# Optimization experiments

Hardware: AMD Instinct MI355X
Metric: run time of the kernel (lower is better)

Reference implementation:

```python
import jax, jax.numpy as jnp
import numpy as np
from jax import lax

C_IN, C_OUT, KH, KW = 8, 8, 3, 3
H, W = 2048, 2048


def setup_inputs() -> dict:
    key = jax.random.key(0)
    k_x, k_w = jax.random.split(key)
    x = jax.random.normal(k_x, (C_IN, H, W), dtype=jnp.float32)
    # kaiming-uniform-ish init, bound = 1/sqrt(fan_in)
    bound = 1.0 / np.sqrt(C_IN * KH * KW)
    weight = jax.random.uniform(k_w, (C_OUT, C_IN, KH, KW), dtype=jnp.float32,
                                minval=-bound, maxval=bound)
    return {"x": x, "weight": weight}


def reference(x, weight):
    # Faithful to Conv2d_mvm_function.forward: valid cross-correlation on a
    # single (C,H,W) image; stride/padding/dilation ignored, bias never added.
    out = lax.conv_general_dilated(
        x[None],                      # (1, C_in, H, W)
        weight,                       # (C_out, C_in, KH, KW)
        window_strides=(1, 1),
        padding="VALID",
        dimension_numbers=("NCHW", "OIHW", "NCHW"),
    )
    return out[0]                     # (C_out, H-KH+1, W-KW+1)
```

## Files before the change

### kernel.cpp

```cpp
#include <hip/hip_runtime.h>


#define H_IN   2048
#define W_IN   2048
#define H_OUT  2046
#define W_OUT  2046
#define CIN    8
#define COUT   8

#define TPR 512
#define NGROUPS 1023
#define PLANE ((size_t)H_IN * W_IN)

__device__ __forceinline__
void load_rows(float (&in)[4][6], const float* __restrict__ base, int ci, bool full) {
    #pragma unroll
    for (int r = 0; r < 4; ++r) {
        const float* p = base + (size_t)ci * PLANE + (size_t)r * W_IN;
        const float4 v4 = *reinterpret_cast<const float4*>(p);
        in[r][0] = v4.x; in[r][1] = v4.y; in[r][2] = v4.z; in[r][3] = v4.w;
        if (full) {
            const float2 v2 = *reinterpret_cast<const float2*>(p + 4);
            in[r][4] = v2.x; in[r][5] = v2.y;
        } else {
            in[r][4] = 0.0f; in[r][5] = 0.0f;
        }
    }
}

__device__ __forceinline__
void compute_ci(float (&acc)[2][COUT][4], const float (&in)[4][6],
                const float* __restrict__ w, int ci) {
    #pragma unroll
    for (int r = 0; r < 4; ++r) {
        #pragma unroll
        for (int co = 0; co < COUT; ++co) {
            #pragma unroll
            for (int kw = 0; kw < 3; ++kw) {
                if (r < 3) {
                    const float wt = w[((co * CIN + ci) * 3 + r) * 3 + kw];
                    #pragma unroll
                    for (int px = 0; px < 4; ++px)
                        acc[0][co][px] = fmaf(wt, in[r][kw + px], acc[0][co][px]);
                }
                if (r >= 1) {
                    const float wt = w[((co * CIN + ci) * 3 + (r - 1)) * 3 + kw];
                    #pragma unroll
                    for (int px = 0; px < 4; ++px)
                        acc[1][co][px] = fmaf(wt, in[r][kw + px], acc[1][co][px]);
                }
            }
        }
    }
}

__global__ __launch_bounds__(256)
void conv3x3_v3(const float* __restrict__ x,
                const float* __restrict__ w,
                float* __restrict__ out) {
    const int gtid = blockIdx.x * 256 + threadIdx.x;
    const int g  = gtid / TPR;
    const int tw = gtid - g * TPR;
    const int oh = g * 2;
    const int ow = tw * 4;
    const bool full = (tw != TPR - 1);

    float acc[2][COUT][4];
    #pragma unroll
    for (int r = 0; r < 2; ++r)
        #pragma unroll
        for (int co = 0; co < COUT; ++co)
            #pragma unroll
            for (int p = 0; p < 4; ++p)
                acc[r][co][p] = 0.0f;

    const float* base = x + (size_t)oh * W_IN + ow;

    float A[4][6], B[4][6];
    load_rows(A, base, 0, full);

    #pragma unroll 1
    for (int k = 0; k < CIN / 2; ++k) {
        const int ci0 = 2 * k;
        const int ci1 = ci0 + 1;

        load_rows(B, base, ci1, full);
        __builtin_amdgcn_sched_barrier(0);
        compute_ci(acc, A, w, ci0);

        if (k < CIN / 2 - 1)
            load_rows(A, base, ci0 + 2, full);
        __builtin_amdgcn_sched_barrier(0);
        compute_ci(acc, B, w, ci1);
    }

    #pragma unroll
    for (int co = 0; co < COUT; ++co) {
        float* o0 = out + ((size_t)co * H_OUT + (size_t)oh) * W_OUT + ow;
        float* o1 = o0 + W_OUT;
        if (full) {
            *reinterpret_cast<float4*>(o0) =
                make_float4(acc[0][co][0], acc[0][co][1], acc[0][co][2], acc[0][co][3]);
            *reinterpret_cast<float2*>(o1)     = make_float2(acc[1][co][0], acc[1][co][1]);
            *reinterpret_cast<float2*>(o1 + 2) = make_float2(acc[1][co][2], acc[1][co][3]);
        } else {
            *reinterpret_cast<float2*>(o0) = make_float2(acc[0][co][0], acc[0][co][1]);
            *reinterpret_cast<float2*>(o1) = make_float2(acc[1][co][0], acc[1][co][1]);
        }
    }
}

extern "C" void kernel_launch(void* const* d_in, const int* in_sizes, int n_in,
                              void* d_out, int out_size, void* d_ws, size_t ws_size,
                              hipStream_t stream) {
    const float* x = (const float*)d_in[0];
    const float* w = (const float*)d_in[1];
    float* out = (float*)d_out;

    const int total_threads = NGROUPS * TPR;
    const int block = 256;
    const int grid = total_threads / block;

    conv3x3_v3<<<grid, block, 0, stream>>>(x, w, out);
}
```

Measured before the change: 278.0 us.

## Stage input rows in LDS via async global_load_lds with double buffering

Each 512-thread block now handles two output rows across the full width. The four input rows per channel are staged into a double-buffered LDS tile with direct global-to-LDS loads, and explicit vmcnt waits plus barriers let the next channel load while the current one is computed. The aim is to replace the overlapping unaligned global float4/float2 reads with coalesced 16-byte async copies and to overlap memory with compute. It adds 64KB of LDS per block, which limits occupancy, and block-wide barrier synchronisation, and it relies on hand-tuned waitcnt counts being correct.

```diff
diff --git a/kernel.cpp b/kernel.cpp
--- a/kernel.cpp
+++ b/kernel.cpp
@@ -1,4 +1,5 @@
 #include <hip/hip_runtime.h>
+#include <stdint.h>
 
 
 #define H_IN   2048
@@ -7,30 +8,29 @@
 #define W_OUT  2046
 #define CIN    8
 #define COUT   8
+#define PLANE  ((size_t)H_IN * W_IN)
 
-#define TPR 512
-#define NGROUPS 1023
-#define PLANE ((size_t)H_IN * W_IN)
+template<int N>
+__device__ __forceinline__ void vm_wait() {
+    asm volatile("s_waitcnt vmcnt(%0)" :: "n"(N) : "memory");
+}
 
 __device__ __forceinline__
-void load_rows(float (&in)[4][6], const float* __restrict__ base, int ci, bool full) {
+void compute_phase(float (&acc)[2][COUT][4],
+                   const float* __restrict__ w, int ci,
+                   const float (&buf)[4][W_IN], int ow, bool full) {
+    float in[4][6];
     #pragma unroll
     for (int r = 0; r < 4; ++r) {
-        const float* p = base + (size_t)ci * PLANE + (size_t)r * W_IN;
-        const float4 v4 = *reinterpret_cast<const float4*>(p);
+        const float4 v4 = *reinterpret_cast<const float4*>(&buf[r][ow]);
         in[r][0] = v4.x; in[r][1] = v4.y; in[r][2] = v4.z; in[r][3] = v4.w;
         if (full) {
-            const float2 v2 = *reinterpret_cast<const float2*>(p + 4);
+            const float2 v2 = *reinterpret_cast<const float2*>(&buf[r][ow + 4]);
             in[r][4] = v2.x; in[r][5] = v2.y;
         } else {
             in[r][4] = 0.0f; in[r][5] = 0.0f;
         }
     }
-}
-
-__device__ __forceinline__
-void compute_ci(float (&acc)[2][COUT][4], const float (&in)[4][6],
-                const float* __restrict__ w, int ci) {
     #pragma unroll
     for (int r = 0; r < 4; ++r) {
         #pragma unroll
@@ -54,16 +54,32 @@
     }
 }
 
-__global__ __launch_bounds__(256)
-void conv3x3_v3(const float* __restrict__ x,
+__global__ __launch_bounds__(512, 4)
+void conv3x3_v4(const float* __restrict__ x,
                 const float* __restrict__ w,
                 float* __restrict__ out) {
-    const int gtid = blockIdx.x * 256 + threadIdx.x;
-    const int g  = gtid / TPR;
-    const int tw = gtid - g * TPR;
-    const int oh = g * 2;
-    const int ow = tw * 4;
-    const bool full = (tw != TPR - 1);
+    __shared__ float lds[2][4][W_IN];
+
+    const int tid  = threadIdx.x;
+    const int wave = tid >> 6;
+    const int lane = tid & 63;
+    const int oh   = blockIdx.x * 2;
+    const int ow   = tid * 4;
+    const bool full = (tid != 511);
+
+#define STAGE(b, ci) do {                                                     \
+        const float* _src = x + (size_t)(ci) * PLANE + (size_t)oh * W_IN;     \
+        _Pragma("unroll")                                                     \
+        for (int _i = 0; _i < 4; ++_i) {                                      \
+            const int _j = wave * 4 + _i;                                     \
+            const int _row = _j >> 3, _chunk = _j & 7;                        \
+            const float* _g = _src + _row * W_IN + _chunk * 256 + lane * 4;   \
+            __builtin_amdgcn_global_load_lds(                                 \
+                (const __attribute__((address_space(1))) uint32_t*)_g,        \
+                (__attribute__((address_space(3))) uint32_t*)&lds[b][_row][_chunk * 256], \
+                16, 0, 0);                                                    \
+        }                                                                     \
+    } while (0)
 
     float acc[2][COUT][4];
     #pragma unroll
@@ -74,25 +90,33 @@
             for (int p = 0; p < 4; ++p)
                 acc[r][co][p] = 0.0f;
 
-    const float* base = x + (size_t)oh * W_IN + ow;
-
-    float A[4][6], B[4][6];
-    load_rows(A, base, 0, full);
+    STAGE(0, 0);
 
     #pragma unroll 1
-    for (int k = 0; k < CIN / 2; ++k) {
-        const int ci0 = 2 * k;
-        const int ci1 = ci0 + 1;
+    for (int k = 0; k < 4; ++k) {
+        const int ci0 = 2 * k, ci1 = 2 * k + 1;
 
-        load_rows(B, base, ci1, full);
+        STAGE(1, ci1);
+        vm_wait<4>();
+        __builtin_amdgcn_s_barrier();
         __builtin_amdgcn_sched_barrier(0);
-        compute_ci(acc, A, w, ci0);
+        compute_phase(acc, w, ci0, lds[0], ow, full);
+        __builtin_amdgcn_sched_barrier(0);
+        __builtin_amdgcn_s_barrier();
 
-        if (k < CIN / 2 - 1)
-            load_rows(A, base, ci0 + 2, full);
+        if (k < 3) {
+            STAGE(0, ci1 + 1);
+            vm_wait<4>();
+        } else {
+            vm_wait<0>();
+        }
+        __builtin_amdgcn_s_barrier();
         __builtin_amdgcn_sched_barrier(0);
-        compute_ci(acc, B, w, ci1);
+        compute_phase(acc, w, ci1, lds[1], ow, full);
+        __builtin_amdgcn_sched_barrier(0);
+        __builtin_amdgcn_s_barrier();
     }
+#undef STAGE
 
     #pragma unroll
     for (int co = 0; co < COUT; ++co) {
@@ -117,9 +141,6 @@
     const float* w = (const float*)d_in[1];
     float* out = (float*)d_out;
 
-    const int total_threads = NGROUPS * TPR;
-    const int block = 256;
-    const int grid = total_threads / block;
-
-    conv3x3_v3<<<grid, block, 0, stream>>>(x, w, out);
+    const int grid = H_OUT / 2;
+    conv3x3_v4<<<grid, 512, 0, stream>>>(x, w, out);
 }
```

New measurement: 301.4 us. 1.08x slower.
